# Optimization experiments

Hardware: AMD Instinct MI355X
Metric: run time of the kernel (lower is better)

The kernel has to match this reference:

```python
import jax, jax.numpy as jnp
import numpy as np

B, S, H = 2, 2048, 2048
NQ, NKV = 32, 8          # query heads, kv heads
G = NQ // NKV            # query groups per kv head
D = H // NQ              # head dim = 64
MAX_POS = 4096
THETA = 10000.0


def _rope_tables(position_ids):
    # freqs per the original apply_rotary_emb (interleaved pair convention)
    freqs = 1.0 / THETA ** (jnp.arange(0, D, 2)[: D // 2].astype(jnp.float32) / D)
    t = jnp.arange(MAX_POS, dtype=jnp.float32)
    ang = jnp.outer(t, freqs)                     # [MAX_POS, D/2]
    cos = jnp.take(jnp.cos(ang), position_ids, axis=0)[:, :, None, :]  # [B,S,1,D/2]
    sin = jnp.take(jnp.sin(ang), position_ids, axis=0)[:, :, None, :]
    return cos, sin


def _apply_rope(x, cos, sin):
    # x: [B,S,h,D]; pairs are interleaved (x0,x1),(x2,x3),...
    x2 = x.astype(jnp.float32).reshape(*x.shape[:-1], D // 2, 2)
    xr, xi = x2[..., 0], x2[..., 1]
    out_r = xr * cos - xi * sin
    out_i = xr * sin + xi * cos
    return jnp.stack((out_r, out_i), axis=-1).reshape(x.shape).astype(x.dtype)


def setup_inputs() -> dict:
    key = jax.random.key(0)
    ks = jax.random.split(key, 5)
    init_scale = 0.02 / np.sqrt(H)
    hidden_states = jax.random.normal(ks[0], (B, S, H), dtype=jnp.float32)
    wq = jax.random.normal(ks[1], (H, H), dtype=jnp.float32) * init_scale
    wk = jax.random.normal(ks[2], (H, H // G), dtype=jnp.float32) * init_scale
    wv = jax.random.normal(ks[3], (H, H // G), dtype=jnp.float32) * init_scale
    wo = jax.random.normal(ks[4], (H, H), dtype=jnp.float32) * init_scale
    attention_mask = jnp.ones((B, S), dtype=jnp.int32)
    position_ids = jnp.broadcast_to(jnp.arange(S, dtype=jnp.int32), (B, S))
    return dict(hidden_states=hidden_states, attention_mask=attention_mask,
                position_ids=position_ids, wq=wq, wk=wk, wv=wv, wo=wo)


def reference(hidden_states, attention_mask, position_ids, wq, wk, wv, wo):
    # projections (no bias)
    xq = (hidden_states @ wq).reshape(B, S, NQ, D)
    xk = (hidden_states @ wk).reshape(B, S, NKV, D)
    xv = (hidden_states @ wv).reshape(B, S, NKV, D)
    # GQA repeat: kv head h -> query heads h*G .. h*G+G-1 (consecutive)
    xk = jnp.repeat(xk, G, axis=2)  # [B,S,NQ,D]
    xv = jnp.repeat(xv, G, axis=2)

    cos, sin = _rope_tables(position_ids)
    xq = _apply_rope(xq, cos, sin)
    xk = _apply_rope(xk, cos, sin)

    # causal + padding mask -> additive bias
    causal = jnp.tril(jnp.ones((S, S), dtype=bool))[None, None]          # [1,1,S,S]
    pad = (attention_mask > 0)[:, None, None, :]                          # [B,1,1,S]
    combined = jnp.logical_and(causal, pad)                               # [B,1,S,S]
    neg = jnp.finfo(jnp.float32).min
    bias = jnp.where(combined, 0.0, neg).astype(jnp.float32)

    scale = 1.0 / np.sqrt(D)
    scores = jnp.einsum('bqhd,bkhd->bhqk', xq, xk).astype(jnp.float32) * scale
    scores = scores + bias
    attn = jax.nn.softmax(scores, axis=-1)                                # [B,NQ,S,S] fp32
    out = jnp.einsum('bhqk,bkhd->bqhd', attn, xv)                         # [B,S,NQ,D]
    out = out.reshape(B, S, H)
    return out @ wo
```

## Files before the change

### kernel.cpp

```cpp
#include <hip/hip_runtime.h>
#include <cstdint>

typedef __attribute__((ext_vector_type(8))) __bf16  bf8v;
typedef __attribute__((ext_vector_type(4))) float   f4v;
typedef __attribute__((ext_vector_type(8))) unsigned short ush8;

__device__ __forceinline__ float bf2f(unsigned short u) {
    union { unsigned u; float f; } v; v.u = ((unsigned)u) << 16; return v.f;
}
__device__ __forceinline__ unsigned short f2bf(float f) {
    union { float f; unsigned u; } v; v.f = f;
    unsigned u = v.u;
    return (unsigned short)((u + 0x7fffu + ((u >> 16) & 1u)) >> 16);
}
__device__ __forceinline__ unsigned short f2bf_n(float f) {
    union { __bf16 h; unsigned short s; } v; v.h = (__bf16)f; return v.s;
}
__device__ __forceinline__ unsigned pack2bf(float a, float b) {
    union { __bf16 h[2]; unsigned u; } v;
    v.h[0] = (__bf16)a; v.h[1] = (__bf16)b; return v.u;
}

#define GLDS16(gp, lp)                                                          \
    __builtin_amdgcn_global_load_lds(                                           \
        (const __attribute__((address_space(1))) void*)(uintptr_t)(gp),         \
        (__attribute__((address_space(3))) void*)(uintptr_t)(lp), 16, 0, 0)

__global__ void cast_f32_to_bf16(const float* __restrict__ in,
                                 unsigned short* __restrict__ out, int n8) {
    int i = blockIdx.x * 256 + threadIdx.x;
    if (i >= n8) return;
    float4 a = ((const float4*)in)[2 * i];
    float4 b = ((const float4*)in)[2 * i + 1];
    ush8 o;
    o[0] = f2bf(a.x); o[1] = f2bf(a.y); o[2] = f2bf(a.z); o[3] = f2bf(a.w);
    o[4] = f2bf(b.x); o[5] = f2bf(b.y); o[6] = f2bf(b.z); o[7] = f2bf(b.w);
    ((ush8*)out)[i] = o;
}

__global__ void transpose_cast(const float* __restrict__ in,
                               unsigned short* __restrict__ out, int R, int C) {
    __shared__ float t[32][33];
    int c0 = blockIdx.x * 32, r0 = blockIdx.y * 32;
    int x = threadIdx.x, y = threadIdx.y;
    #pragma unroll
    for (int i = 0; i < 32; i += 8) t[y + i][x] = in[(size_t)(r0 + y + i) * C + c0 + x];
    __syncthreads();
    #pragma unroll
    for (int i = 0; i < 32; i += 8)
        out[(size_t)(c0 + y + i) * R + r0 + x] = f2bf(t[x][y + i]);
}

__global__ void transpose_v_bf16(const unsigned short* __restrict__ in,
                                 unsigned short* __restrict__ out) {
    __shared__ unsigned short t[32][33];
    int c0 = blockIdx.x * 32;
    int r0 = blockIdx.y * 32;
    int x = threadIdx.x, y = threadIdx.y;
    #pragma unroll
    for (int i = 0; i < 32; i += 8)
        t[y + i][x] = in[(size_t)(r0 + y + i) * 3072 + 2560 + c0 + x];
    __syncthreads();
    #pragma unroll
    for (int i = 0; i < 32; i += 8)
        out[(size_t)(c0 + y + i) * 4096 + r0 + x] = t[x][y + i];
}

__global__ void rope_strided(unsigned short* __restrict__ X,
                             const int* __restrict__ pos_ids,
                             int coloff, int stride, int nh_log2) {
    int idx = blockIdx.x * 256 + threadIdx.x;
    int i   = idx & 31;
    int hh  = (idx >> 5) & ((1 << nh_log2) - 1);
    int tok = idx >> (5 + nh_log2);
    int pos = pos_ids[tok];
    float ang = (float)pos * exp2f(-0.41524101186092f * (float)i);
    float s = sinf(ang), c = cosf(ang);
    unsigned short* p = X + (size_t)tok * stride + coloff + hh * 64 + 2 * i;
    unsigned pr = *(const unsigned*)p;
    float xr = bf2f((unsigned short)(pr & 0xffff));
    float xi = bf2f((unsigned short)(pr >> 16));
    float orr = xr * c - xi * s;
    float oi  = xr * s + xi * c;
    *(unsigned*)p = (unsigned)f2bf(orr) | ((unsigned)f2bf(oi) << 16);
}

template <int OUT_BF16>
__global__ __launch_bounds__(256) void gemm_bt(const unsigned short* __restrict__ A,
                                               const unsigned short* __restrict__ Bt,
                                               void* __restrict__ Cv, int N, int K) {
    __shared__ __align__(16) unsigned short As[128 * 64];
    __shared__ __align__(16) unsigned short Bs[128 * 64];
    const int t = threadIdx.x;
    const int lane = t & 63, w = t >> 6;
    const int wr = w >> 1, wc = w & 1;
    const int lr = lane & 15, lh = lane >> 4;
    const int m0 = blockIdx.y * 128, n0 = blockIdx.x * 128;

    f4v acc[4][4];
    #pragma unroll
    for (int i = 0; i < 4; ++i)
        #pragma unroll
        for (int j = 0; j < 4; ++j) acc[i][j] = f4v{0.f, 0.f, 0.f, 0.f};

    const int o_t = t * 16;
    for (int k0 = 0; k0 < K; k0 += 64) {
        __syncthreads();
        #pragma unroll
        for (int s = 0; s < 4; ++s) {
            int o = s * 4096 + o_t;
            int row = o >> 7;
            int src = (o & 127) ^ ((row & 7) << 4);
            const unsigned short* gA = A + (size_t)(m0 + row) * K + k0 + (src >> 1);
            GLDS16(gA, As + (o >> 1));
            const unsigned short* gB = Bt + (size_t)(n0 + row) * K + k0 + (src >> 1);
            GLDS16(gB, Bs + (o >> 1));
        }
        __syncthreads();
        #pragma unroll
        for (int kk = 0; kk < 2; ++kk) {
            bf8v af[4], bfr[4];
            #pragma unroll
            for (int mi = 0; mi < 4; ++mi) {
                int row = wr * 64 + mi * 16 + lr;
                int col = (kk * 32 + lh * 8) ^ ((row & 7) << 3);
                af[mi] = *(const bf8v*)(As + row * 64 + col);
            }
            #pragma unroll
            for (int ni = 0; ni < 4; ++ni) {
                int row = wc * 64 + ni * 16 + lr;
                int col = (kk * 32 + lh * 8) ^ ((row & 7) << 3);
                bfr[ni] = *(const bf8v*)(Bs + row * 64 + col);
            }
            #pragma unroll
            for (int mi = 0; mi < 4; ++mi)
                #pragma unroll
                for (int ni = 0; ni < 4; ++ni)
                    acc[mi][ni] = __builtin_amdgcn_mfma_f32_16x16x32_bf16(
                        af[mi], bfr[ni], acc[mi][ni], 0, 0, 0);
        }
    }
    #pragma unroll
    for (int mi = 0; mi < 4; ++mi)
        #pragma unroll
        for (int ni = 0; ni < 4; ++ni)
            #pragma unroll
            for (int r = 0; r < 4; ++r) {
                int row = m0 + wr * 64 + mi * 16 + lh * 4 + r;
                int col = n0 + wc * 64 + ni * 16 + lr;
                float v = acc[mi][ni][r];
                if (OUT_BF16) ((unsigned short*)Cv)[(size_t)row * N + col] = f2bf(v);
                else          ((float*)Cv)[(size_t)row * N + col] = v;
            }
}

__global__ __launch_bounds__(256, 4) void flash_attn(
        const unsigned short* __restrict__ QKV,
        const unsigned short* __restrict__ VtG,
        const int* __restrict__ amask,
        unsigned short* __restrict__ O) {
    __shared__ __align__(16) unsigned short Ks[2][64 * 64];
    __shared__ __align__(16) unsigned short Vs[2][64 * 64];
    __shared__ __align__(16) unsigned short Ps[4][16 * 64];

    const int t = threadIdx.x, lane = t & 63, w = t >> 6;
    const int lr = lane & 15, lh = lane >> 4;
    const int pair = blockIdx.x, h = blockIdx.y, b = blockIdx.z;
    const size_t tok0 = (size_t)b * 2048;

    const unsigned short* Kb = QKV + tok0 * 3072 + 2048 + (h >> 2) * 64;
    const unsigned short* Vb = VtG + (size_t)((h >> 2) * 64) * 4096 + tok0;
    const int* amrow = amask + b * 2048;

#define STAGE(buf, kt)                                                              \
    {   _Pragma("unroll")                                                           \
        for (int s_ = 0; s_ < 2; ++s_) {                                            \
            int c_ = s_ * 256 + t;                                                  \
            int row_ = c_ >> 3;                                                     \
            int sc_ = (((c_ & 7) * 16) ^ ((row_ & 7) << 4)) >> 1;                   \
            GLDS16(Kb + (size_t)((kt) * 64 + row_) * 3072 + sc_, Ks[buf] + c_ * 8); \
            GLDS16(Vb + (size_t)row_ * 4096 + (kt) * 64 + sc_, Vs[buf] + c_ * 8);   \
        }                                                                           \
    }

    const float SCL = 0.18033688011112042f;
    int cur = 0;

    #pragma unroll 1
    for (int half = 0; half < 2; ++half) {
        const int qt = half ? (31 - pair) : pair;
        const int q0 = qt * 64;
        const int nkv = qt + 1;
        const int qloc = w * 16 + lr;

        const unsigned short* Qp = QKV + (tok0 + q0 + qloc) * 3072 + h * 64;
        bf8v qa0 = *(const bf8v*)(Qp + lh * 8);
        bf8v qa1 = *(const bf8v*)(Qp + 32 + lh * 8);

        f4v oacc[4];
        #pragma unroll
        for (int i = 0; i < 4; ++i) oacc[i] = f4v{0.f, 0.f, 0.f, 0.f};
        float m_ = -1e30f, l_ = 0.f;

        STAGE(cur, 0);
        __syncthreads();

        #pragma unroll 1
        for (int kt = 0; kt < nkv; ++kt) {
            if (kt + 1 < nkv) STAGE(cur ^ 1, kt + 1);

            int amv[4][4];
            #pragma unroll
            for (int kf = 0; kf < 4; ++kf) {
                int4 aq = *(const int4*)(amrow + kt * 64 + kf * 16 + lh * 4);
                amv[kf][0] = aq.x; amv[kf][1] = aq.y; amv[kf][2] = aq.z; amv[kf][3] = aq.w;
            }

            f4v sa[4];
            #pragma unroll
            for (int kf = 0; kf < 4; ++kf) sa[kf] = f4v{0.f, 0.f, 0.f, 0.f};
            #pragma unroll
            for (int kk = 0; kk < 2; ++kk) {
                bf8v qa = kk ? qa1 : qa0;
                int col = kk * 32 + lh * 8;
                #pragma unroll
                for (int kf = 0; kf < 4; ++kf) {
                    bf8v kb = *(const bf8v*)(Ks[cur] + (kf * 16 + lr) * 64 + (col ^ ((lr & 7) << 3)));
                    sa[kf] = __builtin_amdgcn_mfma_f32_16x16x32_bf16(kb, qa, sa[kf], 0, 0, 0);
                }
            }

            const bool diag = (kt == qt);
            int av = amv[0][0];
            #pragma unroll
            for (int kf = 0; kf < 4; ++kf)
                #pragma unroll
                for (int r = 0; r < 4; ++r) av &= amv[kf][r];
            const bool allAlive = __all(av != 0);

            float pvv[4][4];
            if (allAlive && !diag) {
                #pragma unroll
                for (int kf = 0; kf < 4; ++kf)
                    #pragma unroll
                    for (int r = 0; r < 4; ++r) pvv[kf][r] = sa[kf][r];
            } else {
                #pragma unroll
                for (int kf = 0; kf < 4; ++kf)
                    #pragma unroll
                    for (int r = 0; r < 4; ++r) {
                        int keyl = kf * 16 + lh * 4 + r;
                        bool dead = (amv[kf][r] == 0) || (diag && keyl > qloc);
                        pvv[kf][r] = dead ? -1e30f : sa[kf][r];
                    }
            }

            float t0 = fmaxf(fmaxf(pvv[0][0], pvv[0][1]), fmaxf(pvv[0][2], pvv[0][3]));
            float t1 = fmaxf(fmaxf(pvv[1][0], pvv[1][1]), fmaxf(pvv[1][2], pvv[1][3]));
            float t2 = fmaxf(fmaxf(pvv[2][0], pvv[2][1]), fmaxf(pvv[2][2], pvv[2][3]));
            float t3 = fmaxf(fmaxf(pvv[3][0], pvv[3][1]), fmaxf(pvv[3][2], pvv[3][3]));
            float mx = fmaxf(fmaxf(t0, t1), fmaxf(t2, t3));
            mx = fmaxf(mx, __shfl_xor(mx, 16));
            mx = fmaxf(mx, __shfl_xor(mx, 32));

            float mn = fmaxf(m_, mx * SCL);
            float fac = exp2f(m_ - mn);
            m_ = mn;

            float pe[4][4];
            #pragma unroll
            for (int kf = 0; kf < 4; ++kf)
                #pragma unroll
                for (int r = 0; r < 4; ++r)
                    pe[kf][r] = exp2f(fmaf(pvv[kf][r], SCL, -mn));
            float s0 = (pe[0][0] + pe[0][1]) + (pe[0][2] + pe[0][3]);
            float s1 = (pe[1][0] + pe[1][1]) + (pe[1][2] + pe[1][3]);
            float s2 = (pe[2][0] + pe[2][1]) + (pe[2][2] + pe[2][3]);
            float s3 = (pe[3][0] + pe[3][1]) + (pe[3][2] + pe[3][3]);
            float rs = (s0 + s1) + (s2 + s3);
            rs += __shfl_xor(rs, 16);
            rs += __shfl_xor(rs, 32);
            l_ = l_ * fac + rs;

            float facr[4];
            #pragma unroll
            for (int r = 0; r < 4; ++r) facr[r] = __shfl(fac, lh * 4 + r);
            #pragma unroll
            for (int df = 0; df < 4; ++df) {
                f4v o = oacc[df];
                o[0] *= facr[0]; o[1] *= facr[1]; o[2] *= facr[2]; o[3] *= facr[3];
                oacc[df] = o;
            }

            unsigned short* Pw = Ps[w];
            #pragma unroll
            for (int kf = 0; kf < 4; ++kf) {
                uint2 pk;
                pk.x = pack2bf(pe[kf][0], pe[kf][1]);
                pk.y = pack2bf(pe[kf][2], pe[kf][3]);
                int idx = lr * 64 + ((kf * 16 + lh * 4) ^ ((lr & 7) << 3));
                *(uint2*)(Pw + idx) = pk;
            }

            #pragma unroll
            for (int kk = 0; kk < 2; ++kk) {
                int k0c = kk * 32 + lh * 8;
                bf8v pa = *(const bf8v*)(Pw + lr * 64 + (k0c ^ ((lr & 7) << 3)));
                #pragma unroll
                for (int df = 0; df < 4; ++df) {
                    int d = df * 16 + lr;
                    bf8v vb = *(const bf8v*)(Vs[cur] + d * 64 + (k0c ^ ((d & 7) << 3)));
                    oacc[df] = __builtin_amdgcn_mfma_f32_16x16x32_bf16(pa, vb, oacc[df], 0, 0, 0);
                }
            }

            __syncthreads();
            cur ^= 1;
        }

        float invl = 1.0f / l_;
        float invr[4];
        #pragma unroll
        for (int r = 0; r < 4; ++r) invr[r] = __shfl(invl, lh * 4 + r);
        #pragma unroll
        for (int df = 0; df < 4; ++df)
            #pragma unroll
            for (int r = 0; r < 4; ++r) {
                int qg = q0 + w * 16 + lh * 4 + r;
                float v = oacc[df][r] * invr[r];
                O[(tok0 + qg) * 2048 + h * 64 + df * 16 + lr] = f2bf_n(v);
            }
    }
#undef STAGE
}

extern "C" void kernel_launch(void* const* d_in, const int* in_sizes, int n_in,
                              void* d_out, int out_size, void* d_ws, size_t ws_size,
                              hipStream_t stream) {
    const float* hs   = (const float*)d_in[0];
    const int* amask  = (const int*)d_in[1];
    const int* pos    = (const int*)d_in[2];
    const float* wq   = (const float*)d_in[3];
    const float* wk   = (const float*)d_in[4];
    const float* wv   = (const float*)d_in[5];
    const float* wo   = (const float*)d_in[6];

    char* ws = (char*)d_ws;
    unsigned short* Xb   = (unsigned short*)(ws);
    unsigned short* Wqkv = (unsigned short*)(ws + 16777216);
    unsigned short* Wot  = (unsigned short*)(ws + 29360128);
    unsigned short* AOb  = (unsigned short*)(ws + 37748736);

    char* ob = (char*)d_out;
    unsigned short* QKV = (unsigned short*)ob;
    unsigned short* VtG = (unsigned short*)(ob + 25165824);

    cast_f32_to_bf16<<<4096, 256, 0, stream>>>(hs, Xb, 1048576);
    transpose_cast<<<dim3(64, 64), dim3(32, 8), 0, stream>>>(wq, Wqkv, 2048, 2048);
    transpose_cast<<<dim3(16, 64), dim3(32, 8), 0, stream>>>(wk, Wqkv + 4194304, 2048, 512);
    transpose_cast<<<dim3(16, 64), dim3(32, 8), 0, stream>>>(wv, Wqkv + 5242880, 2048, 512);
    transpose_cast<<<dim3(64, 64), dim3(32, 8), 0, stream>>>(wo, Wot, 2048, 2048);

    gemm_bt<1><<<dim3(24, 32), 256, 0, stream>>>(Xb, Wqkv, (void*)QKV, 3072, 2048);

    rope_strided<<<16384, 256, 0, stream>>>(QKV, pos, 0, 3072, 5);
    rope_strided<<<4096, 256, 0, stream>>>(QKV, pos, 2048, 3072, 3);

    transpose_v_bf16<<<dim3(16, 128), dim3(32, 8), 0, stream>>>(QKV, VtG);

    flash_attn<<<dim3(16, 32, 2), 256, 0, stream>>>(QKV, VtG, amask, AOb);

    gemm_bt<0><<<dim3(16, 32), 256, 0, stream>>>(AOb, Wot, d_out, 2048, 2048);
}
```

Measured before the change: 233.3 us.

## Fuse Q RoPE into attention, precompute tile masks, add lazy rescale and setprio

Removes the separate RoPE kernel for Q and applies rotary embedding and softmax scale in registers when Q is loaded in the attention kernel. Precomputes per-tile padding liveness into shared memory so mask values are only read for tiles that contain padding. Adds lazy online-softmax rescaling, which skips the O rescale unless the max grows by more than a threshold, and raises wave priority around the MFMA blocks. These save a full pass over Q and per-tile mask loads, at the cost of extra sin/cos per block, slight precision differences, and more branches.

Result: slower. 241.6 us (+3.5%).

```diff
diff --git a/kernel.cpp b/kernel.cpp
--- a/kernel.cpp
+++ b/kernel.cpp
@@ -158,10 +158,12 @@
         const unsigned short* __restrict__ QKV,
         const unsigned short* __restrict__ VtG,
         const int* __restrict__ amask,
+        const int* __restrict__ pos_ids,
         unsigned short* __restrict__ O) {
     __shared__ __align__(16) unsigned short Ks[2][64 * 64];
     __shared__ __align__(16) unsigned short Vs[2][64 * 64];
     __shared__ __align__(16) unsigned short Ps[4][16 * 64];
+    __shared__ int aliveT[32];
 
     const int t = threadIdx.x, lane = t & 63, w = t >> 6;
     const int lr = lane & 15, lh = lane >> 4;
@@ -186,6 +188,15 @@
     const float SCL = 0.18033688011112042f;
     int cur = 0;
 
+    if (t < 32) aliveT[t] = -1;
+    __syncthreads();
+    {
+        const int4* am4 = (const int4*)amrow;
+        int4 a0 = am4[2 * t], a1 = am4[2 * t + 1];
+        int f = (a0.x && a0.y && a0.z && a0.w && a1.x && a1.y && a1.z && a1.w) ? -1 : 0;
+        atomicAnd(&aliveT[t >> 3], f);
+    }
+
     #pragma unroll 1
     for (int half = 0; half < 2; ++half) {
         const int qt = half ? (31 - pair) : pair;
@@ -194,8 +205,28 @@
         const int qloc = w * 16 + lr;
 
         const unsigned short* Qp = QKV + (tok0 + q0 + qloc) * 3072 + h * 64;
-        bf8v qa0 = *(const bf8v*)(Qp + lh * 8);
-        bf8v qa1 = *(const bf8v*)(Qp + 32 + lh * 8);
+        union Q8 { bf8v v; unsigned short s[8]; } qa0u, qa1u;
+        qa0u.v = *(const bf8v*)(Qp + lh * 8);
+        qa1u.v = *(const bf8v*)(Qp + 32 + lh * 8);
+        {
+            int pos = pos_ids[tok0 + q0 + qloc];
+            #pragma unroll
+            for (int r = 0; r < 4; ++r) {
+                float i0 = (float)(lh * 4 + r);
+                float ang0 = (float)pos * exp2f(-0.41524101186092f * i0);
+                float sn = sinf(ang0), cs = cosf(ang0);
+                float xr = bf2f(qa0u.s[2 * r]), xi = bf2f(qa0u.s[2 * r + 1]);
+                qa0u.s[2 * r]     = f2bf_n((xr * cs - xi * sn) * SCL);
+                qa0u.s[2 * r + 1] = f2bf_n((xr * sn + xi * cs) * SCL);
+                float i1 = (float)(16 + lh * 4 + r);
+                float ang1 = (float)pos * exp2f(-0.41524101186092f * i1);
+                float sn1 = sinf(ang1), cs1 = cosf(ang1);
+                float yr = bf2f(qa1u.s[2 * r]), yi = bf2f(qa1u.s[2 * r + 1]);
+                qa1u.s[2 * r]     = f2bf_n((yr * cs1 - yi * sn1) * SCL);
+                qa1u.s[2 * r + 1] = f2bf_n((yr * sn1 + yi * cs1) * SCL);
+            }
+        }
+        const bf8v qa0 = qa0u.v, qa1 = qa1u.v;
 
         f4v oacc[4];
         #pragma unroll
@@ -209,16 +240,10 @@
         for (int kt = 0; kt < nkv; ++kt) {
             if (kt + 1 < nkv) STAGE(cur ^ 1, kt + 1);
 
-            int amv[4][4];
-            #pragma unroll
-            for (int kf = 0; kf < 4; ++kf) {
-                int4 aq = *(const int4*)(amrow + kt * 64 + kf * 16 + lh * 4);
-                amv[kf][0] = aq.x; amv[kf][1] = aq.y; amv[kf][2] = aq.z; amv[kf][3] = aq.w;
-            }
-
             f4v sa[4];
             #pragma unroll
             for (int kf = 0; kf < 4; ++kf) sa[kf] = f4v{0.f, 0.f, 0.f, 0.f};
+            __builtin_amdgcn_s_setprio(1);
             #pragma unroll
             for (int kk = 0; kk < 2; ++kk) {
                 bf8v qa = kk ? qa1 : qa0;
@@ -229,22 +254,32 @@
                     sa[kf] = __builtin_amdgcn_mfma_f32_16x16x32_bf16(kb, qa, sa[kf], 0, 0, 0);
                 }
             }
+            __builtin_amdgcn_s_setprio(0);
 
             const bool diag = (kt == qt);
-            int av = amv[0][0];
-            #pragma unroll
-            for (int kf = 0; kf < 4; ++kf)
-                #pragma unroll
-                for (int r = 0; r < 4; ++r) av &= amv[kf][r];
-            const bool allAlive = __all(av != 0);
+            const bool tileAlive = (aliveT[kt] != 0);
 
             float pvv[4][4];
-            if (allAlive && !diag) {
+            if (tileAlive && !diag) {
                 #pragma unroll
                 for (int kf = 0; kf < 4; ++kf)
                     #pragma unroll
                     for (int r = 0; r < 4; ++r) pvv[kf][r] = sa[kf][r];
+            } else if (tileAlive) {
+                #pragma unroll
+                for (int kf = 0; kf < 4; ++kf)
+                    #pragma unroll
+                    for (int r = 0; r < 4; ++r) {
+                        int keyl = kf * 16 + lh * 4 + r;
+                        pvv[kf][r] = (keyl > qloc) ? -1e30f : sa[kf][r];
+                    }
             } else {
+                int amv[4][4];
+                #pragma unroll
+                for (int kf = 0; kf < 4; ++kf) {
+                    int4 aq = *(const int4*)(amrow + kt * 64 + kf * 16 + lh * 4);
+                    amv[kf][0] = aq.x; amv[kf][1] = aq.y; amv[kf][2] = aq.z; amv[kf][3] = aq.w;
+                }
                 #pragma unroll
                 for (int kf = 0; kf < 4; ++kf)
                     #pragma unroll
@@ -263,16 +298,28 @@
             mx = fmaxf(mx, __shfl_xor(mx, 16));
             mx = fmaxf(mx, __shfl_xor(mx, 32));
 
-            float mn = fmaxf(m_, mx * SCL);
-            float fac = exp2f(m_ - mn);
-            m_ = mn;
+            if (!__all(mx <= m_ + 8.0f)) {
+                float mn = fmaxf(m_, mx);
+                float fac = exp2f(m_ - mn);
+                m_ = mn;
+                l_ *= fac;
+                float facr[4];
+                #pragma unroll
+                for (int r = 0; r < 4; ++r) facr[r] = __shfl(fac, lh * 4 + r);
+                #pragma unroll
+                for (int df = 0; df < 4; ++df) {
+                    f4v o = oacc[df];
+                    o[0] *= facr[0]; o[1] *= facr[1]; o[2] *= facr[2]; o[3] *= facr[3];
+                    oacc[df] = o;
+                }
+            }
 
             float pe[4][4];
             #pragma unroll
             for (int kf = 0; kf < 4; ++kf)
                 #pragma unroll
                 for (int r = 0; r < 4; ++r)
-                    pe[kf][r] = exp2f(fmaf(pvv[kf][r], SCL, -mn));
+                    pe[kf][r] = exp2f(pvv[kf][r] - m_);
             float s0 = (pe[0][0] + pe[0][1]) + (pe[0][2] + pe[0][3]);
             float s1 = (pe[1][0] + pe[1][1]) + (pe[1][2] + pe[1][3]);
             float s2 = (pe[2][0] + pe[2][1]) + (pe[2][2] + pe[2][3]);
@@ -280,17 +327,7 @@
             float rs = (s0 + s1) + (s2 + s3);
             rs += __shfl_xor(rs, 16);
             rs += __shfl_xor(rs, 32);
-            l_ = l_ * fac + rs;
-
-            float facr[4];
-            #pragma unroll
-            for (int r = 0; r < 4; ++r) facr[r] = __shfl(fac, lh * 4 + r);
-            #pragma unroll
-            for (int df = 0; df < 4; ++df) {
-                f4v o = oacc[df];
-                o[0] *= facr[0]; o[1] *= facr[1]; o[2] *= facr[2]; o[3] *= facr[3];
-                oacc[df] = o;
-            }
+            l_ += rs;
 
             unsigned short* Pw = Ps[w];
             #pragma unroll
@@ -302,6 +339,7 @@
                 *(uint2*)(Pw + idx) = pk;
             }
 
+            __builtin_amdgcn_s_setprio(1);
             #pragma unroll
             for (int kk = 0; kk < 2; ++kk) {
                 int k0c = kk * 32 + lh * 8;
@@ -313,6 +351,7 @@
                     oacc[df] = __builtin_amdgcn_mfma_f32_16x16x32_bf16(pa, vb, oacc[df], 0, 0, 0);
                 }
             }
+            __builtin_amdgcn_s_setprio(0);
 
             __syncthreads();
             cur ^= 1;
@@ -363,12 +402,11 @@
 
     gemm_bt<1><<<dim3(24, 32), 256, 0, stream>>>(Xb, Wqkv, (void*)QKV, 3072, 2048);
 
-    rope_strided<<<16384, 256, 0, stream>>>(QKV, pos, 0, 3072, 5);
     rope_strided<<<4096, 256, 0, stream>>>(QKV, pos, 2048, 3072, 3);
 
     transpose_v_bf16<<<dim3(16, 128), dim3(32, 8), 0, stream>>>(QKV, VtG);
 
-    flash_attn<<<dim3(16, 32, 2), 256, 0, stream>>>(QKV, VtG, amask, AOb);
+    flash_attn<<<dim3(16, 32, 2), 256, 0, stream>>>(QKV, VtG, amask, pos, AOb);
 
     gemm_bt<0><<<dim3(16, 32), 256, 0, stream>>>(AOb, Wot, d_out, 2048, 2048);
 }
```
